# Kernel tuning notes

Measured on AMD Instinct MI355X. Metric: run time of the kernel, lower is better.

Reference implementation:

```python
import jax, jax.numpy as jnp
import numpy as np

S, N, H, E, V, K = 128, 256, 1024, 512, 32000, 1024  # seq, batch, hidden, embed, vocab, energy channels


def setup_inputs() -> dict:
    key = jax.random.key(0)
    ks = jax.random.split(key, 10)
    s = 0.02
    return {
        "input": jax.random.randint(ks[0], (N,), 0, V),
        "encoder_states": jax.random.normal(ks[1], (S, N, H), jnp.float32),
        "hidden": jax.random.normal(ks[2], (1, N, H), jnp.float32),
        "cell": jax.random.normal(ks[3], (1, N, H), jnp.float32),
        "emb": jax.random.normal(ks[4], (V, E), jnp.float32) * s,
        "W_energy": jax.random.normal(ks[5], (K, 2 * H), jnp.float32) * s,
        "b_energy": jnp.zeros((K,), jnp.float32),
        "W_ih": jax.random.normal(ks[6], (4 * H, H + E), jnp.float32) * s,
        "b_ih": jnp.zeros((4 * H,), jnp.float32),
        "W_hh": jax.random.normal(ks[7], (4 * H, H), jnp.float32) * s,
        "b_hh": jnp.zeros((4 * H,), jnp.float32),
        "W_fc": jax.random.normal(ks[8], (V, H), jnp.float32) * s,
        "b_fc": jnp.zeros((V,), jnp.float32),
    }


def reference(input, encoder_states, hidden, cell, emb, W_energy, b_energy,
              W_ih, b_ih, W_hh, b_hh, W_fc, b_fc):
    seq = encoder_states.shape[0]
    n = encoder_states.shape[1]
    h0 = hidden[0]                                   # [N,H]
    c0 = cell[0]                                     # [N,H]
    emb_x = emb[input]                               # [N,E]

    # additive-attention energy: cat(hidden repeated over S, encoder_states) -> Linear -> ReLU
    h_rep = jnp.broadcast_to(hidden, (seq, n, hidden.shape[2]))
    cat = jnp.concatenate([h_rep, encoder_states], axis=2)          # [S,N,2H]
    energy = jax.nn.relu(jnp.einsum('snh,kh->snk', cat, W_energy) + b_energy)  # [S,N,K]
    # softmax over dim 0 (sequence), independently per (n,k) channel
    attn_last = jax.nn.softmax(energy[..., -1], axis=0)             # [S,N]
    # einsum('snk,snl->knl')[-1] only uses channel k=K-1; contract just that slice
    ctx = jnp.einsum('sn,snl->nl', attn_last, encoder_states)       # [N,H]

    # single-step LSTM (PyTorch gate order i,f,g,o)
    rnn_in = jnp.concatenate([ctx, emb_x], axis=1)                  # [N,H+E]
    gates = rnn_in @ W_ih.T + b_ih + h0 @ W_hh.T + b_hh             # [N,4H]
    i, f, g, o = jnp.split(gates, 4, axis=1)
    c1 = jax.nn.sigmoid(f) * c0 + jax.nn.sigmoid(i) * jnp.tanh(g)
    h1 = jax.nn.sigmoid(o) * jnp.tanh(c1)

    predictions = h1 @ W_fc.T + b_fc                                # [N,V]
    return predictions, h1[None], c1[None]
```

## Files before the change

kernel.cpp:

```cpp
#include <hip/hip_runtime.h>

#define S_DIM 128
#define N_DIM 256
#define H_DIM 1024
#define E_DIM 512
#define V_DIM 32000
#define KE_DIM 1024
#define CIN 2560
#define G4 4096

typedef unsigned short u16;
typedef __bf16 bf16x8 __attribute__((ext_vector_type(8)));
typedef float  f32x4  __attribute__((ext_vector_type(4)));

union U16x8 { uint4 u; bf16x8 b; };

__device__ __forceinline__ unsigned f2bf(float x) {
  unsigned u = __float_as_uint(x);
  return (u + 0x7FFFu + ((u >> 16) & 1u)) >> 16;
}
__device__ __forceinline__ unsigned pk2(float a, float b) {
  return f2bf(a) | (f2bf(b) << 16);
}

__device__ __forceinline__ bf16x8 frag_from_global(const u16* p) {
  U16x8 t; t.u = *(const uint4*)p; return t.b;
}
__device__ __forceinline__ bf16x8 frag_from_lds(const u16* base, int byteoff) {
  U16x8 t; t.u = *(const uint4*)((const char*)base + byteoff); return t.b;
}

__device__ __forceinline__ int loff64(int row, int k) {
  return row * 128 + ((((k >> 3) ^ (row & 7)) << 4) | ((k & 7) << 1));
}
__device__ __forceinline__ int loff128(int row, int k) {
  return row * 256 + ((((k >> 3) ^ (row & 7)) << 4) | ((k & 7) << 1));
}

__device__ __forceinline__ f32x4 mfma16(bf16x8 a, bf16x8 b, f32x4 c) {
  return __builtin_amdgcn_mfma_f32_16x16x32_bf16(a, b, c, 0, 0, 0);
}

__global__ __launch_bounds__(256) void k1_attn(
    const float* __restrict__ enc, const float* __restrict__ hid,
    const float* __restrict__ Wen, const float* __restrict__ ben,
    const int* __restrict__ inp, const float* __restrict__ emb,
    u16* __restrict__ A2)
{
  __shared__ float s_acc[4][H_DIM];
  __shared__ float s_ml[8];
  const int n = blockIdx.x;
  const int t = threadIdx.x;
  const int wave = t >> 6, lane = t & 63;

  const float* Wrow = Wen + (KE_DIM - 1) * (2 * H_DIM);
  float4 we[4];
  #pragma unroll
  for (int ks = 0; ks < 4; ++ks)
    we[ks] = *(const float4*)(Wrow + H_DIM + ks * 256 + lane * 4);

  float hd = 0.f;
  #pragma unroll
  for (int ks = 0; ks < 4; ++ks) {
    float4 wh = *(const float4*)(Wrow + ks * 256 + lane * 4);
    float4 hv = *(const float4*)(hid + n * H_DIM + ks * 256 + lane * 4);
    hd += wh.x * hv.x + wh.y * hv.y + wh.z * hv.z + wh.w * hv.w;
  }
  #pragma unroll
  for (int off = 32; off > 0; off >>= 1) hd += __shfl_xor(hd, off, 64);
  const float ebase = hd + ben[KE_DIM - 1];

  float m = -INFINITY, l = 0.f;
  float4 acc[4];
  #pragma unroll
  for (int ks = 0; ks < 4; ++ks) acc[ks] = make_float4(0.f, 0.f, 0.f, 0.f);

  const long rstride = 4L * N_DIM * H_DIM;
  const float* p = enc + ((long)wave * N_DIM + n) * H_DIM + lane * 4;
  float4 cur[4];
  #pragma unroll
  for (int ks = 0; ks < 4; ++ks) cur[ks] = *(const float4*)(p + ks * 256);

  for (int s = wave; s < S_DIM; s += 4) {
    float4 nxt[4];
    const float* pn = p + rstride;
    const bool has = (s + 4 < S_DIM);
    if (has) {
      #pragma unroll
      for (int ks = 0; ks < 4; ++ks) nxt[ks] = *(const float4*)(pn + ks * 256);
    }
    float d = 0.f;
    #pragma unroll
    for (int ks = 0; ks < 4; ++ks)
      d += we[ks].x * cur[ks].x + we[ks].y * cur[ks].y +
           we[ks].z * cur[ks].z + we[ks].w * cur[ks].w;
    #pragma unroll
    for (int off = 32; off > 0; off >>= 1) d += __shfl_xor(d, off, 64);
    const float e  = fmaxf(ebase + d, 0.f);
    const float nm = fmaxf(m, e);
    const float sc = __expf(m - nm);
    const float pe = __expf(e - nm);
    l = l * sc + pe;
    #pragma unroll
    for (int ks = 0; ks < 4; ++ks) {
      acc[ks].x = acc[ks].x * sc + pe * cur[ks].x;
      acc[ks].y = acc[ks].y * sc + pe * cur[ks].y;
      acc[ks].z = acc[ks].z * sc + pe * cur[ks].z;
      acc[ks].w = acc[ks].w * sc + pe * cur[ks].w;
    }
    m = nm;
    if (has) {
      #pragma unroll
      for (int ks = 0; ks < 4; ++ks) cur[ks] = nxt[ks];
    }
    p = pn;
  }

  #pragma unroll
  for (int ks = 0; ks < 4; ++ks)
    *(float4*)&s_acc[wave][ks * 256 + lane * 4] = acc[ks];
  if (lane == 0) { s_ml[wave] = m; s_ml[4 + wave] = l; }
  __syncthreads();

  const float M = fmaxf(fmaxf(s_ml[0], s_ml[1]), fmaxf(s_ml[2], s_ml[3]));
  const float f0 = __expf(s_ml[0] - M), f1 = __expf(s_ml[1] - M);
  const float f2 = __expf(s_ml[2] - M), f3 = __expf(s_ml[3] - M);
  const float L = s_ml[4] * f0 + s_ml[5] * f1 + s_ml[6] * f2 + s_ml[7] * f3;
  const float invL = 1.0f / L;
  {
    const int e0 = t * 4;
    float v0 = (s_acc[0][e0+0]*f0 + s_acc[1][e0+0]*f1 + s_acc[2][e0+0]*f2 + s_acc[3][e0+0]*f3) * invL;
    float v1 = (s_acc[0][e0+1]*f0 + s_acc[1][e0+1]*f1 + s_acc[2][e0+1]*f2 + s_acc[3][e0+1]*f3) * invL;
    float v2 = (s_acc[0][e0+2]*f0 + s_acc[1][e0+2]*f1 + s_acc[2][e0+2]*f2 + s_acc[3][e0+2]*f3) * invL;
    float v3 = (s_acc[0][e0+3]*f0 + s_acc[1][e0+3]*f1 + s_acc[2][e0+3]*f2 + s_acc[3][e0+3]*f3) * invL;
    uint2 pk; pk.x = pk2(v0, v1); pk.y = pk2(v2, v3);
    *(uint2*)&A2[(long)n * CIN + e0] = pk;
  }

  const int idx = inp[n];
  for (int j = t; j < E_DIM + H_DIM; j += 256) {
    float v = (j < E_DIM) ? emb[(long)idx * E_DIM + j]
                          : hid[n * H_DIM + (j - E_DIM)];
    A2[(long)n * CIN + H_DIM + j] = (u16)f2bf(v);
  }
}

__global__ __launch_bounds__(256) void k2_gates(
    const u16* __restrict__ A2, const float* __restrict__ Wih,
    const float* __restrict__ bih, const float* __restrict__ Whh,
    const float* __restrict__ bhh, float* __restrict__ gates)
{
  __shared__ u16 Blds[16 * 128];
  const int t = threadIdx.x;
  const int wave = t >> 6, lane = t & 63;
  const int quad = lane >> 4, l15 = lane & 15;
  const int j0 = blockIdx.x * 16;
  const int br = t >> 4;
  const int bk = (t & 15) * 8;

  f32x4 acc[4];
  #pragma unroll
  for (int mt = 0; mt < 4; ++mt) acc[mt] = (f32x4){0.f, 0.f, 0.f, 0.f};

  const float* s0 = Wih + (long)(j0 + br) * 1536 + bk;
  float4 v0 = *(const float4*)s0;
  float4 v1 = *(const float4*)(s0 + 4);

  for (int kt = 0; kt < 20; ++kt) {
    const int k0 = kt * 128;
    uint4 pk;
    pk.x = pk2(v0.x, v0.y); pk.y = pk2(v0.z, v0.w);
    pk.z = pk2(v1.x, v1.y); pk.w = pk2(v1.z, v1.w);
    *(uint4*)((char*)Blds + loff128(br, bk)) = pk;
    if (kt + 1 < 20) {
      const int kn = k0 + 128 + bk;
      const float* sn = (kn < 1536) ? (Wih + (long)(j0 + br) * 1536 + kn)
                                    : (Whh + (long)(j0 + br) * 1024 + (kn - 1536));
      v0 = *(const float4*)sn;
      v1 = *(const float4*)(sn + 4);
    }
    __syncthreads();
    #pragma unroll
    for (int kstep = 0; kstep < 4; ++kstep) {
      const int kl = kstep * 32 + quad * 8;
      const bf16x8 bfrag = frag_from_lds(Blds, loff128(l15, kl));
      #pragma unroll
      for (int mt = 0; mt < 4; ++mt) {
        const int row = wave * 64 + mt * 16 + l15;
        const bf16x8 afrag = frag_from_global(A2 + (long)row * CIN + k0 + kl);
        acc[mt] = mfma16(afrag, bfrag, acc[mt]);
      }
    }
    __syncthreads();
  }

  const float bias = bih[j0 + l15] + bhh[j0 + l15];
  #pragma unroll
  for (int mt = 0; mt < 4; ++mt) {
    #pragma unroll
    for (int r = 0; r < 4; ++r) {
      const int row = wave * 64 + mt * 16 + quad * 4 + r;
      gates[(long)row * G4 + j0 + l15] = acc[mt][r] + bias;
    }
  }
}

__global__ __launch_bounds__(256) void k2b_lstm(
    const float* __restrict__ gates, const float* __restrict__ cell,
    float* __restrict__ h1, float* __restrict__ c1, u16* __restrict__ h1b)
{
  const int i = blockIdx.x * 256 + threadIdx.x;
  const int n = i >> 10, h = i & 1023;
  const float* g = gates + (long)n * G4 + h;
  const float gi = g[0], gf = g[1024], gg = g[2048], go = g[3072];
  const float si = 1.f / (1.f + __expf(-gi));
  const float sf = 1.f / (1.f + __expf(-gf));
  const float so = 1.f / (1.f + __expf(-go));
  const float tg = tanhf(gg);
  const float cv = sf * cell[i] + si * tg;
  const float hv = so * tanhf(cv);
  c1[i] = cv;
  h1[i] = hv;
  h1b[i] = (u16)f2bf(hv);
}

__global__ __launch_bounds__(256) void k3_fc(
    const u16* __restrict__ h1b, const float* __restrict__ Wfc,
    const float* __restrict__ bfc, float* __restrict__ out)
{
  __shared__ u16 Blds[64 * 64];
  const int t = threadIdx.x;
  const int wave = t >> 6, lane = t & 63;
  const int quad = lane >> 4, l15 = lane & 15;
  const int j0 = blockIdx.x * 64;
  const int br = t >> 2;
  const int bk = (t & 3) * 16;
  const float* bsrc = Wfc + (long)(j0 + br) * 1024 + bk;

  f32x4 acc[4][4];
  #pragma unroll
  for (int mt = 0; mt < 4; ++mt)
    #pragma unroll
    for (int nt = 0; nt < 4; ++nt) acc[mt][nt] = (f32x4){0.f, 0.f, 0.f, 0.f};

  float4 v0 = *(const float4*)(bsrc);
  float4 v1 = *(const float4*)(bsrc + 4);
  float4 v2 = *(const float4*)(bsrc + 8);
  float4 v3 = *(const float4*)(bsrc + 12);

  for (int kt = 0; kt < 16; ++kt) {
    const int k0 = kt * 64;
    uint4 pa, pb;
    pa.x = pk2(v0.x, v0.y); pa.y = pk2(v0.z, v0.w);
    pa.z = pk2(v1.x, v1.y); pa.w = pk2(v1.z, v1.w);
    pb.x = pk2(v2.x, v2.y); pb.y = pk2(v2.z, v2.w);
    pb.z = pk2(v3.x, v3.y); pb.w = pk2(v3.z, v3.w);
    *(uint4*)((char*)Blds + loff64(br, bk)) = pa;
    *(uint4*)((char*)Blds + loff64(br, bk + 8)) = pb;
    if (kt + 1 < 16) {
      const float* sn = bsrc + (k0 + 64);
      v0 = *(const float4*)(sn);
      v1 = *(const float4*)(sn + 4);
      v2 = *(const float4*)(sn + 8);
      v3 = *(const float4*)(sn + 12);
    }
    __syncthreads();
    #pragma unroll
    for (int kstep = 0; kstep < 2; ++kstep) {
      const int kl = kstep * 32 + quad * 8;
      bf16x8 bfrag[4], afrag[4];
      #pragma unroll
      for (int nt = 0; nt < 4; ++nt)
        bfrag[nt] = frag_from_lds(Blds, loff64(nt * 16 + l15, kl));
      #pragma unroll
      for (int mt = 0; mt < 4; ++mt)
        afrag[mt] = frag_from_global(h1b + (long)(wave * 64 + mt * 16 + l15) * 1024 + k0 + kl);
      #pragma unroll
      for (int mt = 0; mt < 4; ++mt)
        #pragma unroll
        for (int nt = 0; nt < 4; ++nt)
          acc[mt][nt] = mfma16(afrag[mt], bfrag[nt], acc[mt][nt]);
    }
    __syncthreads();
  }

  #pragma unroll
  for (int nt = 0; nt < 4; ++nt) {
    const float bv = bfc[j0 + nt * 16 + l15];
    #pragma unroll
    for (int mt = 0; mt < 4; ++mt) {
      #pragma unroll
      for (int r = 0; r < 4; ++r) {
        const int row = wave * 64 + mt * 16 + quad * 4 + r;
        out[(long)row * V_DIM + j0 + nt * 16 + l15] = acc[mt][nt][r] + bv;
      }
    }
  }
}

extern "C" void kernel_launch(void* const* d_in, const int* in_sizes, int n_in,
                              void* d_out, int out_size, void* d_ws, size_t ws_size,
                              hipStream_t stream) {
  const int*   inp  = (const int*)  d_in[0];
  const float* enc  = (const float*)d_in[1];
  const float* hid  = (const float*)d_in[2];
  const float* cell = (const float*)d_in[3];
  const float* emb  = (const float*)d_in[4];
  const float* Wen  = (const float*)d_in[5];
  const float* ben  = (const float*)d_in[6];
  const float* Wih  = (const float*)d_in[7];
  const float* bih  = (const float*)d_in[8];
  const float* Whh  = (const float*)d_in[9];
  const float* bhh  = (const float*)d_in[10];
  const float* Wfc  = (const float*)d_in[11];
  const float* bfc  = (const float*)d_in[12];

  float* out  = (float*)d_out;
  float* pred = out;
  float* h1   = out + (long)N_DIM * V_DIM;
  float* c1   = h1 + (long)N_DIM * H_DIM;

  char* ws = (char*)d_ws;
  u16*   A2    = (u16*)ws;
  float* gates = (float*)(ws + 1310720);
  u16*   h1b   = (u16*)(ws + 1310720 + 4194304);

  k1_attn <<<N_DIM,            256, 0, stream>>>(enc, hid, Wen, ben, inp, emb, A2);
  k2_gates<<<G4 / 16,          256, 0, stream>>>(A2, Wih, bih, Whh, bhh, gates);
  k2b_lstm<<<(N_DIM*H_DIM)/256,256, 0, stream>>>(gates, cell, h1, c1, h1b);
  k3_fc   <<<V_DIM / 64,       256, 0, stream>>>(h1b, Wfc, bfc, pred);
}
```

Measured before the change: 423.4 us.

## Raise parallelism: more waves in attention, split-K gates, narrower FC tiles

The attention kernel now runs 16 waves per batch row instead of 4, so each wave walks fewer sequence steps, and the partial softmax states are merged across 16 waves. The gates GEMM is split into two K halves across twice as many 512-thread blocks, writing two partial buffers that the LSTM kernel sums together with the biases. The FC kernel uses 32-column tiles, doubling the block count. The goal is more concurrent waves and blocks on a GPU that was underfilled, at the cost of extra partial-sum traffic, a larger shared-memory footprint in the attention kernel, and less reuse per FC tile.

```diff
diff --git a/kernel.cpp b/kernel.cpp
--- a/kernel.cpp
+++ b/kernel.cpp
@@ -41,14 +41,14 @@
   return __builtin_amdgcn_mfma_f32_16x16x32_bf16(a, b, c, 0, 0, 0);
 }
 
-__global__ __launch_bounds__(256) void k1_attn(
+__global__ __launch_bounds__(1024, 4) void k1_attn(
     const float* __restrict__ enc, const float* __restrict__ hid,
     const float* __restrict__ Wen, const float* __restrict__ ben,
     const int* __restrict__ inp, const float* __restrict__ emb,
     u16* __restrict__ A2)
 {
-  __shared__ float s_acc[4][H_DIM];
-  __shared__ float s_ml[8];
+  __shared__ float s_acc[16][H_DIM];
+  __shared__ float s_ml[32];
   const int n = blockIdx.x;
   const int t = threadIdx.x;
   const int wave = t >> 6, lane = t & 63;
@@ -75,16 +75,16 @@
   #pragma unroll
   for (int ks = 0; ks < 4; ++ks) acc[ks] = make_float4(0.f, 0.f, 0.f, 0.f);
 
-  const long rstride = 4L * N_DIM * H_DIM;
+  const long rstride = 16L * N_DIM * H_DIM;
   const float* p = enc + ((long)wave * N_DIM + n) * H_DIM + lane * 4;
   float4 cur[4];
   #pragma unroll
   for (int ks = 0; ks < 4; ++ks) cur[ks] = *(const float4*)(p + ks * 256);
 
-  for (int s = wave; s < S_DIM; s += 4) {
+  for (int s = wave; s < S_DIM; s += 16) {
     float4 nxt[4];
     const float* pn = p + rstride;
-    const bool has = (s + 4 < S_DIM);
+    const bool has = (s + 16 < S_DIM);
     if (has) {
       #pragma unroll
       for (int ks = 0; ks < 4; ++ks) nxt[ks] = *(const float4*)(pn + ks * 256);
@@ -119,65 +119,63 @@
   #pragma unroll
   for (int ks = 0; ks < 4; ++ks)
     *(float4*)&s_acc[wave][ks * 256 + lane * 4] = acc[ks];
-  if (lane == 0) { s_ml[wave] = m; s_ml[4 + wave] = l; }
+  if (lane == 0) { s_ml[wave] = m; s_ml[16 + wave] = l; }
   __syncthreads();
 
-  const float M = fmaxf(fmaxf(s_ml[0], s_ml[1]), fmaxf(s_ml[2], s_ml[3]));
-  const float f0 = __expf(s_ml[0] - M), f1 = __expf(s_ml[1] - M);
-  const float f2 = __expf(s_ml[2] - M), f3 = __expf(s_ml[3] - M);
-  const float L = s_ml[4] * f0 + s_ml[5] * f1 + s_ml[6] * f2 + s_ml[7] * f3;
+  float M = -INFINITY;
+  #pragma unroll
+  for (int w = 0; w < 16; ++w) M = fmaxf(M, s_ml[w]);
+  float f[16], L = 0.f;
+  #pragma unroll
+  for (int w = 0; w < 16; ++w) { f[w] = __expf(s_ml[w] - M); L += s_ml[16 + w] * f[w]; }
   const float invL = 1.0f / L;
   {
-    const int e0 = t * 4;
-    float v0 = (s_acc[0][e0+0]*f0 + s_acc[1][e0+0]*f1 + s_acc[2][e0+0]*f2 + s_acc[3][e0+0]*f3) * invL;
-    float v1 = (s_acc[0][e0+1]*f0 + s_acc[1][e0+1]*f1 + s_acc[2][e0+1]*f2 + s_acc[3][e0+1]*f3) * invL;
-    float v2 = (s_acc[0][e0+2]*f0 + s_acc[1][e0+2]*f1 + s_acc[2][e0+2]*f2 + s_acc[3][e0+2]*f3) * invL;
-    float v3 = (s_acc[0][e0+3]*f0 + s_acc[1][e0+3]*f1 + s_acc[2][e0+3]*f2 + s_acc[3][e0+3]*f3) * invL;
-    uint2 pk; pk.x = pk2(v0, v1); pk.y = pk2(v2, v3);
-    *(uint2*)&A2[(long)n * CIN + e0] = pk;
+    float v = 0.f;
+    #pragma unroll
+    for (int w = 0; w < 16; ++w) v += s_acc[w][t] * f[w];
+    A2[(long)n * CIN + t] = (u16)f2bf(v * invL);
   }
 
   const int idx = inp[n];
-  for (int j = t; j < E_DIM + H_DIM; j += 256) {
+  for (int j = t; j < E_DIM + H_DIM; j += 1024) {
     float v = (j < E_DIM) ? emb[(long)idx * E_DIM + j]
                           : hid[n * H_DIM + (j - E_DIM)];
     A2[(long)n * CIN + H_DIM + j] = (u16)f2bf(v);
   }
 }
 
-__global__ __launch_bounds__(256) void k2_gates(
+__global__ __launch_bounds__(512) void k2_gates(
     const u16* __restrict__ A2, const float* __restrict__ Wih,
-    const float* __restrict__ bih, const float* __restrict__ Whh,
-    const float* __restrict__ bhh, float* __restrict__ gates)
+    const float* __restrict__ Whh, float* __restrict__ gp0,
+    float* __restrict__ gp1)
 {
   __shared__ u16 Blds[16 * 128];
   const int t = threadIdx.x;
   const int wave = t >> 6, lane = t & 63;
   const int quad = lane >> 4, l15 = lane & 15;
-  const int j0 = blockIdx.x * 16;
-  const int br = t >> 4;
-  const int bk = (t & 15) * 8;
-
-  f32x4 acc[4];
-  #pragma unroll
-  for (int mt = 0; mt < 4; ++mt) acc[mt] = (f32x4){0.f, 0.f, 0.f, 0.f};
-
-  const float* s0 = Wih + (long)(j0 + br) * 1536 + bk;
-  float4 v0 = *(const float4*)s0;
-  float4 v1 = *(const float4*)(s0 + 4);
-
-  for (int kt = 0; kt < 20; ++kt) {
-    const int k0 = kt * 128;
-    uint4 pk;
-    pk.x = pk2(v0.x, v0.y); pk.y = pk2(v0.z, v0.w);
-    pk.z = pk2(v1.x, v1.y); pk.w = pk2(v1.z, v1.w);
-    *(uint4*)((char*)Blds + loff128(br, bk)) = pk;
-    if (kt + 1 < 20) {
+  const int j0 = (blockIdx.x >> 1) * 16;
+  const int khalf = blockIdx.x & 1;
+  const int kbase = khalf * 1280;
+  const int br = t >> 5;
+  const int bk = (t & 31) * 4;
+
+  f32x4 acc[2];
+  acc[0] = (f32x4){0.f, 0.f, 0.f, 0.f};
+  acc[1] = (f32x4){0.f, 0.f, 0.f, 0.f};
+
+  const long jrow = j0 + br;
+  const float* s0 = Wih + jrow * 1536 + kbase + bk;
+  float4 v = *(const float4*)s0;
+
+  for (int kt = 0; kt < 10; ++kt) {
+    const int k0 = kbase + kt * 128;
+    uint2 pk; pk.x = pk2(v.x, v.y); pk.y = pk2(v.z, v.w);
+    *(uint2*)((char*)Blds + loff128(br, bk)) = pk;
+    if (kt + 1 < 10) {
       const int kn = k0 + 128 + bk;
-      const float* sn = (kn < 1536) ? (Wih + (long)(j0 + br) * 1536 + kn)
-                                    : (Whh + (long)(j0 + br) * 1024 + (kn - 1536));
-      v0 = *(const float4*)sn;
-      v1 = *(const float4*)(sn + 4);
+      const float* sn = (kn < 1536) ? (Wih + jrow * 1536 + kn)
+                                    : (Whh + jrow * 1024 + (kn - 1536));
+      v = *(const float4*)sn;
     }
     __syncthreads();
     #pragma unroll
@@ -185,8 +183,8 @@
       const int kl = kstep * 32 + quad * 8;
       const bf16x8 bfrag = frag_from_lds(Blds, loff128(l15, kl));
       #pragma unroll
-      for (int mt = 0; mt < 4; ++mt) {
-        const int row = wave * 64 + mt * 16 + l15;
+      for (int mt = 0; mt < 2; ++mt) {
+        const int row = wave * 32 + mt * 16 + l15;
         const bf16x8 afrag = frag_from_global(A2 + (long)row * CIN + k0 + kl);
         acc[mt] = mfma16(afrag, bfrag, acc[mt]);
       }
@@ -194,25 +192,30 @@
     __syncthreads();
   }
 
-  const float bias = bih[j0 + l15] + bhh[j0 + l15];
-  #pragma unroll
-  for (int mt = 0; mt < 4; ++mt) {
+  float* gp = khalf ? gp1 : gp0;
+  #pragma unroll
+  for (int mt = 0; mt < 2; ++mt) {
     #pragma unroll
     for (int r = 0; r < 4; ++r) {
-      const int row = wave * 64 + mt * 16 + quad * 4 + r;
-      gates[(long)row * G4 + j0 + l15] = acc[mt][r] + bias;
+      const int row = wave * 32 + mt * 16 + quad * 4 + r;
+      gp[(long)row * G4 + j0 + l15] = acc[mt][r];
     }
   }
 }
 
 __global__ __launch_bounds__(256) void k2b_lstm(
-    const float* __restrict__ gates, const float* __restrict__ cell,
+    const float* __restrict__ gp0, const float* __restrict__ gp1,
+    const float* __restrict__ bih, const float* __restrict__ bhh,
+    const float* __restrict__ cell,
     float* __restrict__ h1, float* __restrict__ c1, u16* __restrict__ h1b)
 {
   const int i = blockIdx.x * 256 + threadIdx.x;
   const int n = i >> 10, h = i & 1023;
-  const float* g = gates + (long)n * G4 + h;
-  const float gi = g[0], gf = g[1024], gg = g[2048], go = g[3072];
+  const long base = (long)n * G4 + h;
+  const float gi = gp0[base]        + gp1[base]        + bih[h]        + bhh[h];
+  const float gf = gp0[base + 1024] + gp1[base + 1024] + bih[h + 1024] + bhh[h + 1024];
+  const float gg = gp0[base + 2048] + gp1[base + 2048] + bih[h + 2048] + bhh[h + 2048];
+  const float go = gp0[base + 3072] + gp1[base + 3072] + bih[h + 3072] + bhh[h + 3072];
   const float si = 1.f / (1.f + __expf(-gi));
   const float sf = 1.f / (1.f + __expf(-gf));
   const float so = 1.f / (1.f + __expf(-go));
@@ -228,49 +231,42 @@
     const u16* __restrict__ h1b, const float* __restrict__ Wfc,
     const float* __restrict__ bfc, float* __restrict__ out)
 {
-  __shared__ u16 Blds[64 * 64];
+  __shared__ u16 Blds[32 * 64];
   const int t = threadIdx.x;
   const int wave = t >> 6, lane = t & 63;
   const int quad = lane >> 4, l15 = lane & 15;
-  const int j0 = blockIdx.x * 64;
-  const int br = t >> 2;
-  const int bk = (t & 3) * 16;
+  const int j0 = blockIdx.x * 32;
+  const int br = t >> 3;
+  const int bk = (t & 7) * 8;
   const float* bsrc = Wfc + (long)(j0 + br) * 1024 + bk;
 
-  f32x4 acc[4][4];
+  f32x4 acc[4][2];
   #pragma unroll
   for (int mt = 0; mt < 4; ++mt)
     #pragma unroll
-    for (int nt = 0; nt < 4; ++nt) acc[mt][nt] = (f32x4){0.f, 0.f, 0.f, 0.f};
+    for (int nt = 0; nt < 2; ++nt) acc[mt][nt] = (f32x4){0.f, 0.f, 0.f, 0.f};
 
   float4 v0 = *(const float4*)(bsrc);
   float4 v1 = *(const float4*)(bsrc + 4);
-  float4 v2 = *(const float4*)(bsrc + 8);
-  float4 v3 = *(const float4*)(bsrc + 12);
 
   for (int kt = 0; kt < 16; ++kt) {
     const int k0 = kt * 64;
-    uint4 pa, pb;
+    uint4 pa;
     pa.x = pk2(v0.x, v0.y); pa.y = pk2(v0.z, v0.w);
     pa.z = pk2(v1.x, v1.y); pa.w = pk2(v1.z, v1.w);
-    pb.x = pk2(v2.x, v2.y); pb.y = pk2(v2.z, v2.w);
-    pb.z = pk2(v3.x, v3.y); pb.w = pk2(v3.z, v3.w);
     *(uint4*)((char*)Blds + loff64(br, bk)) = pa;
-    *(uint4*)((char*)Blds + loff64(br, bk + 8)) = pb;
     if (kt + 1 < 16) {
       const float* sn = bsrc + (k0 + 64);
       v0 = *(const float4*)(sn);
       v1 = *(const float4*)(sn + 4);
-      v2 = *(const float4*)(sn + 8);
-      v3 = *(const float4*)(sn + 12);
     }
     __syncthreads();
     #pragma unroll
     for (int kstep = 0; kstep < 2; ++kstep) {
       const int kl = kstep * 32 + quad * 8;
-      bf16x8 bfrag[4], afrag[4];
-      #pragma unroll
-      for (int nt = 0; nt < 4; ++nt)
+      bf16x8 bfrag[2], afrag[4];
+      #pragma unroll
+      for (int nt = 0; nt < 2; ++nt)
         bfrag[nt] = frag_from_lds(Blds, loff64(nt * 16 + l15, kl));
       #pragma unroll
       for (int mt = 0; mt < 4; ++mt)
@@ -278,14 +274,14 @@
       #pragma unroll
       for (int mt = 0; mt < 4; ++mt)
         #pragma unroll
-        for (int nt = 0; nt < 4; ++nt)
+        for (int nt = 0; nt < 2; ++nt)
           acc[mt][nt] = mfma16(afrag[mt], bfrag[nt], acc[mt][nt]);
     }
     __syncthreads();
   }
 
   #pragma unroll
-  for (int nt = 0; nt < 4; ++nt) {
+  for (int nt = 0; nt < 2; ++nt) {
     const float bv = bfc[j0 + nt * 16 + l15];
     #pragma unroll
     for (int mt = 0; mt < 4; ++mt) {
@@ -322,11 +318,12 @@
 
   char* ws = (char*)d_ws;
   u16*   A2    = (u16*)ws;
-  float* gates = (float*)(ws + 1310720);
-  u16*   h1b   = (u16*)(ws + 1310720 + 4194304);
-
-  k1_attn <<<N_DIM,            256, 0, stream>>>(enc, hid, Wen, ben, inp, emb, A2);
-  k2_gates<<<G4 / 16,          256, 0, stream>>>(A2, Wih, bih, Whh, bhh, gates);
-  k2b_lstm<<<(N_DIM*H_DIM)/256,256, 0, stream>>>(gates, cell, h1, c1, h1b);
-  k3_fc   <<<V_DIM / 64,       256, 0, stream>>>(h1b, Wfc, bfc, pred);
-}
+  float* gp0   = (float*)(ws + 1310720);
+  float* gp1   = (float*)(ws + 1310720 + 4194304);
+  u16*   h1b   = (u16*)(ws + 1310720 + 2 * 4194304);
+
+  k1_attn <<<N_DIM,             1024, 0, stream>>>(enc, hid, Wen, ben, inp, emb, A2);
+  k2_gates<<<(G4 / 16) * 2,      512, 0, stream>>>(A2, Wih, Whh, gp0, gp1);
+  k2b_lstm<<<(N_DIM*H_DIM)/256,  256, 0, stream>>>(gp0, gp1, bih, bhh, cell, h1, c1, h1b);
+  k3_fc   <<<V_DIM / 32,         256, 0, stream>>>(h1b, Wfc, bfc, pred);
+}
```

Result: slower. 434.9 us (+2.7%).
